# Performance work log

Measured on AMD Instinct MI355X. Metric: run time of the kernel, lower is better.

## Reference

```python
import jax, jax.numpy as jnp
import numpy as np

B, S, D = 4, 2048, 1024
H = 16
HD = D // H

def setup_inputs() -> dict:
    key = jax.random.key(0)
    ks = jax.random.split(key, 5)
    x = jax.random.normal(ks[0], (B, S, D), dtype=jnp.float32)
    # PyTorch Linear: y = x @ W.T + b; store W in torch layout [out, in]
    w_qkv = jax.random.normal(ks[1], (3 * D, D), dtype=jnp.float32) * (1.0 / np.sqrt(D))
    b_qkv = jax.random.normal(ks[2], (3 * D,), dtype=jnp.float32) * 0.01
    w_out = jax.random.normal(ks[3], (D, D), dtype=jnp.float32) * (1.0 / np.sqrt(D))
    b_out = jax.random.normal(ks[4], (D,), dtype=jnp.float32) * 0.01
    return {"x": x, "w_qkv": w_qkv, "b_qkv": b_qkv, "w_out": w_out, "b_out": b_out}

def reference(x, w_qkv, b_qkv, w_out, b_out):
    b, s, d = x.shape
    qkv = x @ w_qkv.T + b_qkv                      # [B,S,3D]
    q, k, v = jnp.split(qkv, 3, axis=2)
    # [B,S,D] -> [B,H,S,HD]
    q = q.reshape(b, s, H, HD).transpose(0, 2, 1, 3)
    k = k.reshape(b, s, H, HD).transpose(0, 2, 1, 3)
    v = v.reshape(b, s, H, HD).transpose(0, 2, 1, 3)
    att = jnp.einsum('bhqd,bhkd->bhqk', q, k) / np.sqrt(HD)
    causal = jnp.tril(jnp.ones((s, s), dtype=bool))
    att = jnp.where(causal[None, None], att, -jnp.inf)
    att = jax.nn.softmax(att, axis=-1)
    y = jnp.einsum('bhqk,bhkd->bhqd', att, v)      # [B,H,S,HD]
    y = y.transpose(0, 2, 1, 3).reshape(b, s, d)
    return y @ w_out.T + b_out
```

## Files before the change

kernel.cpp:

```cpp
#include <hip/hip_runtime.h>
#include <hip/hip_bf16.h>

#define DEV __device__ __forceinline__

typedef __attribute__((ext_vector_type(8))) short bf16x8;
typedef __attribute__((ext_vector_type(4))) float f32x4;

#define BB 4
#define SS 2048
#define DD 1024
#define HH 16
#define HDD 64
#define MM (BB * SS)
#define NT (SS / 64)

DEV short f2bf(float f) {
  unsigned u = __builtin_bit_cast(unsigned, f);
  u = u + 0x7fffu + ((u >> 16) & 1u);
  return (short)(u >> 16);
}

DEV float fexp2(float x) {
  float r;
  asm("v_exp_f32 %0, %1" : "=v"(r) : "v"(x));
  return r;
}
DEV float frcp(float x) {
  float r;
  asm("v_rcp_f32 %0, %1" : "=v"(r) : "v"(x));
  return r;
}
DEV unsigned cvtpk(float a, float b) {
  unsigned r;
  asm("v_cvt_pk_bf16_f32 %0, %1, %2" : "=v"(r) : "v"(a), "v"(b));
  return r;
}

DEV void gload_lds16(const void* g, void* l) {
  __builtin_amdgcn_global_load_lds((const __attribute__((address_space(1))) void*)g,
                                   (__attribute__((address_space(3))) void*)l, 16, 0, 0);
}

DEV void cast_range(const float* __restrict__ in, unsigned long long* __restrict__ out,
                    int n4, int start, int stride) {
  for (int i = start; i < n4; i += stride) {
    const float4 f = ((const float4*)in)[i];
    unsigned long long a = (unsigned long long)(unsigned short)f2bf(f.x)
        | ((unsigned long long)(unsigned short)f2bf(f.y) << 16)
        | ((unsigned long long)(unsigned short)f2bf(f.z) << 32)
        | ((unsigned long long)(unsigned short)f2bf(f.w) << 48);
    out[i] = a;
  }
}

__global__ __launch_bounds__(256)
void cast3_f32_bf16(const float* __restrict__ x, unsigned long long* __restrict__ ox, int nx4,
                    const float* __restrict__ wq, unsigned long long* __restrict__ owq, int nwq4,
                    const float* __restrict__ wo, unsigned long long* __restrict__ owo, int nwo4) {
  const int start = blockIdx.x * 256 + threadIdx.x;
  const int stride = gridDim.x * 256;
  cast_range(x, ox, nx4, start, stride);
  cast_range(wq, owq, nwq4, start, stride);
  cast_range(wo, owo, nwo4, start, stride);
}

template<int EPI>
__global__ __launch_bounds__(256)
void gemm_bt(const short* __restrict__ A, const short* __restrict__ Bw,
             const float* __restrict__ bias,
             short* __restrict__ qo, short* __restrict__ ko, short* __restrict__ vo,
             float* __restrict__ co,
             int M, int N, int K) {
  __shared__ short sA[128 * 64];
  __shared__ short sB[128 * 64];
  const int lane = threadIdx.x & 63;
  const int wv = threadIdx.x >> 6;
  const int wm = wv >> 1, wn = wv & 1;
  const int m0 = blockIdx.y * 128;
  const int n0 = blockIdx.x * 128;
  f32x4 acc[4][4] = {};
  const int nkt = K >> 6;
  for (int kt = 0; kt < nkt; ++kt) {
    const int k0 = kt << 6;
    if (kt) __syncthreads();
#pragma unroll
    for (int i = 0; i < 4; ++i) {
      const int c = i * 4 + wv;
      const int b = c * 1024 + lane * 16;
      const int row = b >> 7;
      const int colb = b & 127;
      gload_lds16((const char*)A + ((size_t)(m0 + row) * K + k0) * 2 + colb,
                  (char*)sA + c * 1024);
      gload_lds16((const char*)Bw + ((size_t)(n0 + row) * K + k0) * 2 + colb,
                  (char*)sB + c * 1024);
    }
    __syncthreads();
#pragma unroll
    for (int ks = 0; ks < 2; ++ks) {
      bf16x8 af[4], bf_[4];
#pragma unroll
      for (int i = 0; i < 4; ++i) {
        af[i]  = *(const bf16x8*)&sA[(wm * 64 + i * 16 + (lane & 15)) * 64 + ks * 32 + (lane >> 4) * 8];
        bf_[i] = *(const bf16x8*)&sB[(wn * 64 + i * 16 + (lane & 15)) * 64 + ks * 32 + (lane >> 4) * 8];
      }
#pragma unroll
      for (int i = 0; i < 4; ++i)
#pragma unroll
        for (int j = 0; j < 4; ++j)
          acc[i][j] = __builtin_amdgcn_mfma_f32_16x16x32_bf16(af[i], bf_[j], acc[i][j], 0, 0, 0);
    }
  }
#pragma unroll
  for (int i = 0; i < 4; ++i) {
#pragma unroll
    for (int j = 0; j < 4; ++j) {
#pragma unroll
      for (int r = 0; r < 4; ++r) {
        const int row = m0 + wm * 64 + i * 16 + (lane >> 4) * 4 + r;
        const int col = n0 + wn * 64 + j * 16 + (lane & 15);
        float v = acc[i][j][r] + bias[col];
        if (EPI == 0) {
          const int part = col >> 10, oo = col & 1023;
          const int h = oo >> 6, d = oo & 63;
          const int bb = row >> 11, s = row & 2047;
          if (part == 0)
            qo[(((size_t)bb * HH + h) * SS + s) * HDD + d] = f2bf(v * 0.18033688f);
          else if (part == 1)
            ko[(((size_t)bb * HH + h) * SS + s) * HDD + d] = f2bf(v);
          else {
            const int q = (s >> 2) & 15;
            const int tau = (q & 8) | ((q & 3) << 1) | ((q >> 2) & 1);
            vo[(((size_t)bb * HH + h) * HDD + d) * SS + (s & ~63) + (tau << 2) + (s & 3)] = f2bf(v);
          }
        } else {
          co[(size_t)row * N + col] = v;
        }
      }
    }
  }
}

__global__ __launch_bounds__(256)
void attn_fwd(const short* __restrict__ Q, const short* __restrict__ K,
              const short* __restrict__ V, short* __restrict__ Y) {
  __shared__ short sK[2][64 * 64];
  __shared__ short sV[2][64 * 64];
  const int bh = blockIdx.y;
  const int tid = threadIdx.x, lane = tid & 63, w = tid >> 6;
  const size_t bqk = (size_t)bh * (SS * HDD);
  const size_t bv  = (size_t)bh * (HDD * SS);
  const int b = bh >> 4, h = bh & 15;
  const int lr = lane & 15;
  const int lg = lane >> 4;
  const int lm = lr & 7;

  const int e0 = w * 64 + lane;
  const int e1 = 256 + e0;
  const int r0 = e0 >> 3, s0 = ((e0 & 7) ^ (r0 & 7)) * 8;
  const int r1 = e1 >> 3, s1 = ((e1 & 7) ^ (r1 & 7)) * 8;

  for (int qsel = 0; qsel < 2; ++qsel) {
    const int qb = qsel ? (NT - 1 - blockIdx.x) : blockIdx.x;
    const int q0 = qb * 64;

    __syncthreads();

    {
      const short* gK = K + bqk;
      const short* gV = V + bv;
      gload_lds16(gK + (size_t)r0 * HDD + s0, &sK[0][e0 * 8]);
      gload_lds16(gV + (size_t)r0 * SS + s0, &sV[0][e0 * 8]);
      gload_lds16(gK + (size_t)r1 * HDD + s1, &sK[0][e1 * 8]);
      gload_lds16(gV + (size_t)r1 * SS + s1, &sV[0][e1 * 8]);
    }

    bf16x8 qf[2];
#pragma unroll
    for (int ks = 0; ks < 2; ++ks)
      qf[ks] = *(const bf16x8*)&Q[bqk + (size_t)(q0 + w * 16 + lr) * HDD + ks * 32 + lg * 8];

    f32x4 accO[4] = {};
    float m_ = -1e30f, l_ = 0.f;

    int cur = 0;
    for (int kt = 0; kt <= qb; ++kt) {
      const int kc0 = kt * 64;
      __syncthreads();
      if (kt < qb) {
        const short* gK = K + bqk + (size_t)(kc0 + 64) * 64;
        const short* gV = V + bv + kc0 + 64;
        gload_lds16(gK + (size_t)r0 * HDD + s0, &sK[cur ^ 1][e0 * 8]);
        gload_lds16(gV + (size_t)r0 * SS + s0, &sV[cur ^ 1][e0 * 8]);
        gload_lds16(gK + (size_t)r1 * HDD + s1, &sK[cur ^ 1][e1 * 8]);
        gload_lds16(gV + (size_t)r1 * SS + s1, &sV[cur ^ 1][e1 * 8]);
      }

      f32x4 st_[4] = {};
#pragma unroll
      for (int ks = 0; ks < 2; ++ks) {
#pragma unroll
        for (int nf = 0; nf < 4; ++nf) {
          const int row = nf * 16 + lr;
          const bf16x8 kf = *(const bf16x8*)&sK[cur][row * 64 + (((ks << 2) + lg) ^ lm) * 8];
          st_[nf] = __builtin_amdgcn_mfma_f32_16x16x32_bf16(kf, qf[ks], st_[nf], 0, 0, 0);
        }
      }
      if (kt == qb) {
        const int q = q0 + w * 16 + lr;
#pragma unroll
        for (int nf = 0; nf < 4; ++nf)
#pragma unroll
          for (int r = 0; r < 4; ++r) {
            const int k = kc0 + nf * 16 + lg * 4 + r;
            if (k > q) st_[nf][r] = -1e30f;
          }
      }

      f32x4 t01, t23;
#pragma unroll
      for (int r = 0; r < 4; ++r) {
        t01[r] = fmaxf(st_[0][r], st_[1][r]);
        t23[r] = fmaxf(st_[2][r], st_[3][r]);
      }
      float rm = -1e30f;
#pragma unroll
      for (int r = 0; r < 4; ++r) rm = fmaxf(rm, fmaxf(t01[r], t23[r]));
      rm = fmaxf(rm, __shfl_xor(rm, 16));
      rm = fmaxf(rm, __shfl_xor(rm, 32));

      const bool need = rm > m_ + 11.5416f;
      if (__any(need)) {
        const float mn = fmaxf(m_, rm);
        const float scale = fexp2(m_ - mn);
        m_ = mn;
        l_ *= scale;
#pragma unroll
        for (int r = 0; r < 4; ++r) {
          const float scl = __shfl(scale, (lane & 48) + (lg << 2) + r);
#pragma unroll
          for (int df = 0; df < 4; ++df) accO[df][r] *= scl;
        }
      }

      float rs = 0.f;
#pragma unroll
      for (int nf = 0; nf < 4; ++nf)
#pragma unroll
        for (int r = 0; r < 4; ++r) {
          const float p = fexp2(st_[nf][r] - m_);
          st_[nf][r] = p;
          rs += p;
        }
      rs += __shfl_xor(rs, 16);
      rs += __shfl_xor(rs, 32);
      l_ += rs;

      unsigned u[4][2];
#pragma unroll
      for (int nf = 0; nf < 4; ++nf) {
        u[nf][0] = cvtpk(st_[nf][0], st_[nf][1]);
        u[nf][1] = cvtpk(st_[nf][2], st_[nf][3]);
      }

#pragma unroll
      for (int c = 0; c < 2; ++c) {
        int4 pw;
        pw.x = (int)u[2 * c][0];
        pw.y = (int)u[2 * c][1];
        pw.z = (int)u[2 * c + 1][0];
        pw.w = (int)u[2 * c + 1][1];
        const bf16x8 pf = __builtin_bit_cast(bf16x8, pw);
        const int slot = (((c << 2) + lg) ^ lm) * 8;
#pragma unroll
        for (int df = 0; df < 4; ++df) {
          const bf16x8 vf = *(const bf16x8*)&sV[cur][(df * 16 + lr) * 64 + slot];
          accO[df] = __builtin_amdgcn_mfma_f32_16x16x32_bf16(pf, vf, accO[df], 0, 0, 0);
        }
      }
      cur ^= 1;
    }

#pragma unroll
    for (int r = 0; r < 4; ++r) {
      const float lv = __shfl(l_, (lane & 48) + (lg << 2) + r);
      const float inv = frcp(lv);
      const int srow = q0 + w * 16 + lg * 4 + r;
#pragma unroll
      for (int df = 0; df < 4; ++df) {
        const int dcol = h * HDD + df * 16 + lr;
        Y[((size_t)b * SS + srow) * DD + dcol] = f2bf(accO[df][r] * inv);
      }
    }
  }
}

extern "C" void kernel_launch(void* const* d_in, const int* in_sizes, int n_in,
                              void* d_out, int out_size, void* d_ws, size_t ws_size,
                              hipStream_t stream) {
  const float* x     = (const float*)d_in[0];
  const float* w_qkv = (const float*)d_in[1];
  const float* b_qkv = (const float*)d_in[2];
  const float* w_out = (const float*)d_in[3];
  const float* b_out = (const float*)d_in[4];
  float* out = (float*)d_out;

  const size_t nx = (size_t)MM * DD;
  const size_t nwq = (size_t)3 * DD * DD;
  const size_t nwo = (size_t)DD * DD;

  short* x_bf    = (short*)d_ws;
  short* wqkv_bf = x_bf + nx;
  short* wout_bf = wqkv_bf + nwq;
  short* q_ws    = wout_bf + nwo;
  short* k_ws    = q_ws + nx;
  short* v_ws    = k_ws + nx;
  short* y_ws    = v_ws + nx;

  cast3_f32_bf16<<<dim3(2048), dim3(256), 0, stream>>>(
      x, (unsigned long long*)x_bf, (int)(nx / 4),
      w_qkv, (unsigned long long*)wqkv_bf, (int)(nwq / 4),
      w_out, (unsigned long long*)wout_bf, (int)(nwo / 4));

  gemm_bt<0><<<dim3(3 * DD / 128, MM / 128), dim3(256), 0, stream>>>(
      x_bf, wqkv_bf, b_qkv, q_ws, k_ws, v_ws, nullptr, MM, 3 * DD, DD);

  attn_fwd<<<dim3(NT / 2, BB * HH), dim3(256), 0, stream>>>(q_ws, k_ws, v_ws, y_ws);

  gemm_bt<1><<<dim3(DD / 128, MM / 128), dim3(256), 0, stream>>>(
      y_ws, wout_bf, b_out, nullptr, nullptr, nullptr, out, MM, DD, DD);
}
```

Baseline: 222.1 us.

## Process 128-query tiles per workgroup with two row groups per wave

The attention kernel now assigns 128 query rows per workgroup, with each wave computing two 16-row groups against every K/V tile loaded into LDS. This doubles the MFMA work per shared-memory K/V load and halves the number of K/V tile loads and barriers per query row. Causal masking now covers the last two KV tiles, and the grid is halved. In exchange it uses more registers and launches fewer blocks, which may reduce occupancy and latency hiding.

```diff
diff --git a/kernel.cpp b/kernel.cpp
--- a/kernel.cpp
+++ b/kernel.cpp
@@ -13,6 +13,7 @@
 #define HDD 64
 #define MM (BB * SS)
 #define NT (SS / 64)
+#define NQT (SS / 128)
 
 DEV short f2bf(float f) {
   unsigned u = __builtin_bit_cast(unsigned, f);
@@ -160,8 +161,9 @@
   const int r1 = e1 >> 3, s1 = ((e1 & 7) ^ (r1 & 7)) * 8;
 
   for (int qsel = 0; qsel < 2; ++qsel) {
-    const int qb = qsel ? (NT - 1 - blockIdx.x) : blockIdx.x;
-    const int q0 = qb * 64;
+    const int qt = qsel ? (NQT - 1 - blockIdx.x) : blockIdx.x;
+    const int q0 = qt * 128;
+    const int nkv = 2 * qt + 2;
 
     __syncthreads();
 
@@ -174,19 +176,22 @@
       gload_lds16(gV + (size_t)r1 * SS + s1, &sV[0][e1 * 8]);
     }
 
-    bf16x8 qf[2];
-#pragma unroll
-    for (int ks = 0; ks < 2; ++ks)
-      qf[ks] = *(const bf16x8*)&Q[bqk + (size_t)(q0 + w * 16 + lr) * HDD + ks * 32 + lg * 8];
-
-    f32x4 accO[4] = {};
-    float m_ = -1e30f, l_ = 0.f;
+    const int qbase = q0 + w * 32;
+    bf16x8 qf[2][2];
+#pragma unroll
+    for (int g = 0; g < 2; ++g)
+#pragma unroll
+      for (int ks = 0; ks < 2; ++ks)
+        qf[g][ks] = *(const bf16x8*)&Q[bqk + (size_t)(qbase + g * 16 + lr) * HDD + ks * 32 + lg * 8];
+
+    f32x4 accO[2][4] = {};
+    float m_[2] = {-1e30f, -1e30f}, l_[2] = {0.f, 0.f};
 
     int cur = 0;
-    for (int kt = 0; kt <= qb; ++kt) {
+    for (int kt = 0; kt < nkv; ++kt) {
       const int kc0 = kt * 64;
       __syncthreads();
-      if (kt < qb) {
+      if (kt < nkv - 1) {
         const short* gK = K + bqk + (size_t)(kc0 + 64) * 64;
         const short* gV = V + bv + kc0 + 64;
         gload_lds16(gK + (size_t)r0 * HDD + s0, &sK[cur ^ 1][e0 * 8]);
@@ -195,102 +200,108 @@
         gload_lds16(gV + (size_t)r1 * SS + s1, &sV[cur ^ 1][e1 * 8]);
       }
 
-      f32x4 st_[4] = {};
+      f32x4 st[2][4] = {};
 #pragma unroll
       for (int ks = 0; ks < 2; ++ks) {
 #pragma unroll
         for (int nf = 0; nf < 4; ++nf) {
           const int row = nf * 16 + lr;
           const bf16x8 kf = *(const bf16x8*)&sK[cur][row * 64 + (((ks << 2) + lg) ^ lm) * 8];
-          st_[nf] = __builtin_amdgcn_mfma_f32_16x16x32_bf16(kf, qf[ks], st_[nf], 0, 0, 0);
-        }
-      }
-      if (kt == qb) {
-        const int q = q0 + w * 16 + lr;
+          st[0][nf] = __builtin_amdgcn_mfma_f32_16x16x32_bf16(kf, qf[0][ks], st[0][nf], 0, 0, 0);
+          st[1][nf] = __builtin_amdgcn_mfma_f32_16x16x32_bf16(kf, qf[1][ks], st[1][nf], 0, 0, 0);
+        }
+      }
+      if (kt >= nkv - 2) {
+#pragma unroll
+        for (int g = 0; g < 2; ++g) {
+          const int q = qbase + g * 16 + lr;
+#pragma unroll
+          for (int nf = 0; nf < 4; ++nf)
+#pragma unroll
+            for (int r = 0; r < 4; ++r) {
+              const int k = kc0 + nf * 16 + lg * 4 + r;
+              if (k > q) st[g][nf][r] = -1e30f;
+            }
+        }
+      }
+
+      unsigned u[2][4][2];
+#pragma unroll
+      for (int g = 0; g < 2; ++g) {
+        float rm = -1e30f;
+#pragma unroll
+        for (int r = 0; r < 4; ++r)
+          rm = fmaxf(rm, fmaxf(fmaxf(st[g][0][r], st[g][1][r]), fmaxf(st[g][2][r], st[g][3][r])));
+        rm = fmaxf(rm, __shfl_xor(rm, 16));
+        rm = fmaxf(rm, __shfl_xor(rm, 32));
+
+        const bool need = rm > m_[g] + 11.5416f;
+        if (__any(need)) {
+          const float mn = fmaxf(m_[g], rm);
+          const float scale = fexp2(m_[g] - mn);
+          m_[g] = mn;
+          l_[g] *= scale;
+#pragma unroll
+          for (int r = 0; r < 4; ++r) {
+            const float scl = __shfl(scale, (lane & 48) + (lg << 2) + r);
+#pragma unroll
+            for (int df = 0; df < 4; ++df) accO[g][df][r] *= scl;
+          }
+        }
+
+        float rs = 0.f;
 #pragma unroll
         for (int nf = 0; nf < 4; ++nf)
 #pragma unroll
           for (int r = 0; r < 4; ++r) {
-            const int k = kc0 + nf * 16 + lg * 4 + r;
-            if (k > q) st_[nf][r] = -1e30f;
+            const float p = fexp2(st[g][nf][r] - m_[g]);
+            st[g][nf][r] = p;
+            rs += p;
           }
-      }
-
-      f32x4 t01, t23;
-#pragma unroll
-      for (int r = 0; r < 4; ++r) {
-        t01[r] = fmaxf(st_[0][r], st_[1][r]);
-        t23[r] = fmaxf(st_[2][r], st_[3][r]);
-      }
-      float rm = -1e30f;
-#pragma unroll
-      for (int r = 0; r < 4; ++r) rm = fmaxf(rm, fmaxf(t01[r], t23[r]));
-      rm = fmaxf(rm, __shfl_xor(rm, 16));
-      rm = fmaxf(rm, __shfl_xor(rm, 32));
-
-      const bool need = rm > m_ + 11.5416f;
-      if (__any(need)) {
-        const float mn = fmaxf(m_, rm);
-        const float scale = fexp2(m_ - mn);
-        m_ = mn;
-        l_ *= scale;
-#pragma unroll
-        for (int r = 0; r < 4; ++r) {
-          const float scl = __shfl(scale, (lane & 48) + (lg << 2) + r);
-#pragma unroll
-          for (int df = 0; df < 4; ++df) accO[df][r] *= scl;
-        }
-      }
-
-      float rs = 0.f;
-#pragma unroll
-      for (int nf = 0; nf < 4; ++nf)
-#pragma unroll
-        for (int r = 0; r < 4; ++r) {
-          const float p = fexp2(st_[nf][r] - m_);
-          st_[nf][r] = p;
-          rs += p;
-        }
-      rs += __shfl_xor(rs, 16);
-      rs += __shfl_xor(rs, 32);
-      l_ += rs;
-
-      unsigned u[4][2];
-#pragma unroll
-      for (int nf = 0; nf < 4; ++nf) {
-        u[nf][0] = cvtpk(st_[nf][0], st_[nf][1]);
-        u[nf][1] = cvtpk(st_[nf][2], st_[nf][3]);
+        rs += __shfl_xor(rs, 16);
+        rs += __shfl_xor(rs, 32);
+        l_[g] += rs;
+
+#pragma unroll
+        for (int nf = 0; nf < 4; ++nf) {
+          u[g][nf][0] = cvtpk(st[g][nf][0], st[g][nf][1]);
+          u[g][nf][1] = cvtpk(st[g][nf][2], st[g][nf][3]);
+        }
       }
 
 #pragma unroll
       for (int c = 0; c < 2; ++c) {
-        int4 pw;
-        pw.x = (int)u[2 * c][0];
-        pw.y = (int)u[2 * c][1];
-        pw.z = (int)u[2 * c + 1][0];
-        pw.w = (int)u[2 * c + 1][1];
-        const bf16x8 pf = __builtin_bit_cast(bf16x8, pw);
+        int4 pw0, pw1;
+        pw0.x = (int)u[0][2 * c][0]; pw0.y = (int)u[0][2 * c][1];
+        pw0.z = (int)u[0][2 * c + 1][0]; pw0.w = (int)u[0][2 * c + 1][1];
+        pw1.x = (int)u[1][2 * c][0]; pw1.y = (int)u[1][2 * c][1];
+        pw1.z = (int)u[1][2 * c + 1][0]; pw1.w = (int)u[1][2 * c + 1][1];
+        const bf16x8 pf0 = __builtin_bit_cast(bf16x8, pw0);
+        const bf16x8 pf1 = __builtin_bit_cast(bf16x8, pw1);
         const int slot = (((c << 2) + lg) ^ lm) * 8;
 #pragma unroll
         for (int df = 0; df < 4; ++df) {
           const bf16x8 vf = *(const bf16x8*)&sV[cur][(df * 16 + lr) * 64 + slot];
-          accO[df] = __builtin_amdgcn_mfma_f32_16x16x32_bf16(pf, vf, accO[df], 0, 0, 0);
+          accO[0][df] = __builtin_amdgcn_mfma_f32_16x16x32_bf16(pf0, vf, accO[0][df], 0, 0, 0);
+          accO[1][df] = __builtin_amdgcn_mfma_f32_16x16x32_bf16(pf1, vf, accO[1][df], 0, 0, 0);
         }
       }
       cur ^= 1;
     }
 
 #pragma unroll
-    for (int r = 0; r < 4; ++r) {
-      const float lv = __shfl(l_, (lane & 48) + (lg << 2) + r);
-      const float inv = frcp(lv);
-      const int srow = q0 + w * 16 + lg * 4 + r;
-#pragma unroll
-      for (int df = 0; df < 4; ++df) {
-        const int dcol = h * HDD + df * 16 + lr;
-        Y[((size_t)b * SS + srow) * DD + dcol] = f2bf(accO[df][r] * inv);
-      }
-    }
+    for (int g = 0; g < 2; ++g)
+#pragma unroll
+      for (int r = 0; r < 4; ++r) {
+        const float lv = __shfl(l_[g], (lane & 48) + (lg << 2) + r);
+        const float inv = frcp(lv);
+        const int srow = qbase + g * 16 + lg * 4 + r;
+#pragma unroll
+        for (int df = 0; df < 4; ++df) {
+          const int dcol = h * HDD + df * 16 + lr;
+          Y[((size_t)b * SS + srow) * DD + dcol] = f2bf(accO[g][df][r] * inv);
+        }
+      }
   }
 }
 
@@ -324,7 +335,7 @@
   gemm_bt<0><<<dim3(3 * DD / 128, MM / 128), dim3(256), 0, stream>>>(
       x_bf, wqkv_bf, b_qkv, q_ws, k_ws, v_ws, nullptr, MM, 3 * DD, DD);
 
-  attn_fwd<<<dim3(NT / 2, BB * HH), dim3(256), 0, stream>>>(q_ws, k_ws, v_ws, y_ws);
+  attn_fwd<<<dim3(NQT / 2, BB * HH), dim3(256), 0, stream>>>(q_ws, k_ws, v_ws, y_ws);
 
   gemm_bt<1><<<dim3(DD / 128, MM / 128), dim3(256), 0, stream>>>(
       y_ws, wout_bf, b_out, nullptr, nullptr, nullptr, out, MM, DD, DD);
```

Result: faster. 200.6 us (-9.7%).
